# Kernel optimization log

Measured on AMD Instinct MI355X. Metric: run time of the kernel, lower is better.

The kernel has to match this reference:

```python
import jax, jax.numpy as jnp
import numpy as np

N_E = 1024
E_DIM = 64
BETA = 0.4
N_TOK = 131072


def setup_inputs() -> dict:
    key = jax.random.key(0)
    k1, k2 = jax.random.split(key)
    z = jax.random.normal(k1, (N_TOK, E_DIM), dtype=jnp.float32)
    # torch init: uniform(-1/n_e, 1/n_e)
    codebook = jax.random.uniform(k2, (N_E, E_DIM), dtype=jnp.float32,
                                  minval=-1.0 / N_E, maxval=1.0 / N_E)
    return {"z": z, "codebook": codebook}


def reference(z, codebook):
    sg = jax.lax.stop_gradient
    # squared euclidean distances: [N, n_e]
    d = (jnp.sum(z * z, axis=1, keepdims=True)
         + jnp.sum(codebook * codebook, axis=1)
         - 2.0 * jnp.matmul(z, codebook.T))
    idx = jnp.argmin(d, axis=1)                      # [N]
    z_q = codebook[idx]                              # gather, [N, E_DIM]
    # commitment / codebook loss
    vq_loss = (jnp.mean((sg(z_q) - z) ** 2)
               + BETA * jnp.mean((z_q - sg(z)) ** 2))
    # straight-through estimator
    z_q_st = z + sg(z_q - z)
    # codebook usage statistics (mean of one-hot encodings)
    e_mean = jnp.bincount(idx, length=N_E).astype(z.dtype) / jnp.asarray(idx.shape[0], z.dtype)
    usage_loss = -jnp.sum(e_mean * jnp.log(e_mean + 1e-10))
    perplexity = jnp.exp(usage_loss)
    vq_loss = vq_loss + 0.01 * usage_loss
    return z_q_st, vq_loss, idx[:, None], perplexity
```

## Files before the change

kernel.cpp:

```cpp
#include <hip/hip_runtime.h>
#include <math.h>

#define N_TOK 131072
#define N_E   1024
#define E_DIM 64
#define BETA  0.4

#define ZQ_OFF   0
#define LOSS_OFF 8388608
#define IDX_OFF  8388609
#define PERP_OFF 8519681

#define WS_SLOTS 0
#define WS_C2    2048
#define WS_CNT   6144
#define WS_WLC   10240
#define WS_WLB   10256
#define WS_KEYSB 43024
#define WLCAP    8192

typedef _Float16 f16x8 __attribute__((ext_vector_type(8)));
typedef float f32x4  __attribute__((ext_vector_type(4)));
typedef unsigned long long u64;

__device__ __forceinline__ unsigned med3u(unsigned a, unsigned b, unsigned c) {
    unsigned d;
    asm("v_med3_u32 %0, %1, %2, %3" : "=v"(d) : "v"(a), "v"(b), "v"(c));
    return d;
}

__device__ __attribute__((noinline)) int exact_best_serial2(
    const float* __restrict__ z, const float* __restrict__ cb, int n) {
    const float* zr = z + (size_t)n * E_DIM;
    float r8[8];
#pragma unroll
    for (int j = 0; j < 8; ++j) r8[j] = __fmul_rn(zr[j], zr[j]);
#pragma unroll 1
    for (int i = 8; i < 64; i += 8)
#pragma unroll
        for (int j = 0; j < 8; ++j)
            r8[j] = __fadd_rn(r8[j], __fmul_rn(zr[i + j], zr[i + j]));
    float z2 = __fadd_rn(__fadd_rn(__fadd_rn(r8[0], r8[1]), __fadd_rn(r8[2], r8[3])),
                         __fadd_rn(__fadd_rn(r8[4], r8[5]), __fadd_rn(r8[6], r8[7])));
    u64 bestkey = ~0ull;
#pragma unroll 1
    for (int e = 0; e < N_E; ++e) {
        const float* cp = cb + (size_t)e * E_DIM;
        double cs = 0.0, mm = 0.0;
#pragma unroll 1
        for (int i = 0; i < E_DIM; ++i) {
            double cc = (double)cp[i];
            cs = fma(cc, cc, cs);
            mm = fma((double)zr[i], cc, mm);
        }
        float d = __fsub_rn(__fadd_rn(z2, (float)cs), __fmul_rn(2.0f, (float)mm));
        u64 key = ((u64)__float_as_uint(d) << 32) | (unsigned)e;
        if (key < bestkey) bestkey = key;
    }
    return (int)(bestkey & 0xffffffffu);
}

__global__ __launch_bounds__(1024, 4) void vq_all(
    const float* __restrict__ z, const float* __restrict__ cb,
    double* __restrict__ slots, float* __restrict__ c2g,
    int* __restrict__ counts, int* __restrict__ wlCnt,
    int* __restrict__ wlB, u64* __restrict__ keysB,
    float margin_u, float* __restrict__ out) {

    __shared__ __align__(16) unsigned char sbuf[131072];
    __shared__ __align__(8)  unsigned short c2s[N_E];
    __shared__ int   best_s[512];
    __shared__ unsigned char flag_s[512];
    __shared__ unsigned listA[512];
    __shared__ unsigned short listB[512];
    __shared__ int cntA, cntB, gbaseS;
    __shared__ int hist[N_E];
    __shared__ double wred[16], dredA[16];

    const int tid  = threadIdx.x;
    const int lane = tid & 63;
    const int wid  = tid >> 6;
    const int col  = lane & 15;
    const int quad = lane >> 4;
    const int blk_tok0 = blockIdx.x * 512;
    const int wave_tok0 = blk_tok0 + wid * 32;

    if (tid == 0) { cntA = 0; cntB = 0; }
    hist[tid] = 0;

    float4 zl[2][4];
#pragma unroll
    for (int m = 0; m < 2; ++m) {
        const float* zr = z + (size_t)(wave_tok0 + m * 16 + col) * E_DIM + quad * 8;
#pragma unroll
        for (int kc = 0; kc < 2; ++kc) {
            zl[m][kc * 2]     = *(const float4*)(zr + kc * 32);
            zl[m][kc * 2 + 1] = *(const float4*)(zr + kc * 32 + 4);
        }
    }

    {
        const float4* cb4 = (const float4*)cb;
#pragma unroll
        for (int r = 0; r < 16; ++r) {
            const int ft = r * 1024 + tid;
            const float4 v = cb4[ft];
            const int code = ft >> 4;
            const int k0   = (ft & 15) * 4;
            const int cc = ((code >> 4) << 1) | (k0 >> 5);
            const int l  = (((k0 >> 3) & 3) << 4) | (code & 15);
            const int dst = (cc << 9) | (l << 3) | (k0 & 7);
            union { _Float16 h[4]; uint2 u; } pk;
            pk.h[0] = (_Float16)(v.x * 1024.0f);
            pk.h[1] = (_Float16)(v.y * 1024.0f);
            pk.h[2] = (_Float16)(v.z * 1024.0f);
            pk.h[3] = (_Float16)(v.w * 1024.0f);
            *(uint2*)(sbuf + dst * 2) = pk.u;
        }
    }

    if (blockIdx.x == 0) {
        const float* p = cb + (size_t)tid * E_DIM;
        double s = 0.0;
#pragma unroll
        for (int k = 0; k < E_DIM; ++k) {
            double c = (double)p[k];
            s = fma(c, c, s);
        }
        c2g[tid] = (float)s;
    }
    __syncthreads();

    {
        const int code = tid;
        const int cc0 = (code >> 4) << 1;
        const int c15 = code & 15;
        float s = 0.f;
#pragma unroll
        for (int half = 0; half < 2; ++half)
#pragma unroll
            for (int lv = 0; lv < 4; ++lv) {
                const int off = (((cc0 + half) << 9) |
                                 (((lv << 4) | c15) << 3)) * 2;
                union { uint4 u; _Float16 h[8]; } b;
                b.u = *(const uint4*)(sbuf + off);
#pragma unroll
                for (int j = 0; j < 8; ++j) {
                    float f = (float)b.h[j];
                    s = fmaf(f, f, s);
                }
            }
        union { _Float16 h; unsigned short u; } q;
        q.h = (_Float16)(s * (-1.0f / 2048.0f));
        c2s[tid] = q.u;
    }

    f16x8 Ah[2][2];
#pragma unroll
    for (int m = 0; m < 2; ++m)
#pragma unroll
        for (int kc = 0; kc < 2; ++kc) {
            float4 u0 = zl[m][kc * 2], u1 = zl[m][kc * 2 + 1];
            f16x8 a;
            a[0] = (_Float16)u0.x; a[1] = (_Float16)u0.y;
            a[2] = (_Float16)u0.z; a[3] = (_Float16)u0.w;
            a[4] = (_Float16)u1.x; a[5] = (_Float16)u1.y;
            a[6] = (_Float16)u1.z; a[7] = (_Float16)u1.w;
            Ah[m][kc] = a;
        }

    unsigned k1[2][4], k2[2][4], k3[2][4];
#pragma unroll
    for (int m = 0; m < 2; ++m)
#pragma unroll
        for (int r = 0; r < 4; ++r) { k1[m][r] = 0u; k2[m][r] = 0u; k3[m][r] = 0u; }

    __syncthreads();

#pragma unroll 4
    for (int cl = 0; cl < 64; ++cl) {
        const unsigned char* bp = sbuf + cl * 2048 + lane * 16;
        union { uint4 u; f16x8 v; } b0, b1;
        b0.u = *(const uint4*)(bp);
        b1.u = *(const uint4*)(bp + 1024);
        union { unsigned short us; _Float16 h; } cv;
        cv.us = c2s[cl * 16 + col];
        const float ch = 64.0f + (float)cv.h;
        const f32x4 cinit = {ch, ch, ch, ch};
        const unsigned ctag = (unsigned)(63 - cl);
#pragma unroll
        for (int m = 0; m < 2; ++m) {
            f32x4 acc = __builtin_amdgcn_mfma_f32_16x16x32_f16(
                Ah[m][0], b0.v, cinit, 0, 0, 0);
            acc = __builtin_amdgcn_mfma_f32_16x16x32_f16(
                Ah[m][1], b1.v, acc, 0, 0, 0);
#pragma unroll
            for (int r = 0; r < 4; ++r) {
                unsigned key = (__float_as_uint(acc[r]) & 0xFFFFFFC0u) | ctag;
                unsigned t1 = min(k1[m][r], key);
                k3[m][r] = med3u(k2[m][r], k3[m][r], t1);
                k2[m][r] = med3u(k1[m][r], k2[m][r], key);
                k1[m][r] = max(k1[m][r], key);
            }
        }
    }

#pragma unroll 1
    for (int m = 0; m < 2; ++m) {
#pragma unroll 1
        for (int r = 0; r < 4; ++r) {
            const unsigned l1 = k1[m][r], l2 = k2[m][r], l3 = k3[m][r];
            unsigned g1 = l1, g2 = l2, g3 = l3;
#pragma unroll
            for (int d = 1; d < 16; d <<= 1) {
                unsigned p1 = __shfl_xor(g1, d, 64);
                unsigned p2 = __shfl_xor(g2, d, 64);
                unsigned p3 = __shfl_xor(g3, d, 64);
                unsigned t1 = min(g1, p1);
                g3 = med3u(g2, g3, t1);
                g2 = med3u(g1, g2, p1);
                g1 = max(g1, p1);
                g3 = med3u(g2, g3, p2);
                g2 = max(g2, p2);
                g3 = med3u(g2, g3, p3);
            }
            u64 bal1 = __ballot((l1 == g1) || (l2 == g1) || (l3 == g1));
            u64 bal2 = __ballot((l1 == g2) || (l2 == g2) || (l3 == g2));
            if (col == 0) {
                const int tl = wid * 32 + m * 16 + quad * 4 + r;
                unsigned m1 = (unsigned)((bal1 >> (quad * 16)) & 0xFFFFu);
                int c1 = __ffs(m1) - 1;
                int bbest = (63 - (int)(g1 & 63u)) * 16 + c1;
                float v1 = __uint_as_float(g1 & 0xFFFFFFC0u);
                float v2 = __uint_as_float(g2 & 0xFFFFFFC0u);
                float v3 = __uint_as_float(g3 & 0xFFFFFFC0u);
                int typ = 0, bsec = 0;
                if (v1 - v2 < margin_u) {
                    if (v1 - v3 < margin_u) typ = 2;
                    else {
                        unsigned m2 = (unsigned)((bal2 >> (quad * 16)) & 0xFFFFu);
                        if (g2 == g1) m2 &= ~(1u << c1);
                        if (__popc(m2) == 1) {
                            bsec = (63 - (int)(g2 & 63u)) * 16 + (__ffs(m2) - 1);
                            typ = 1;
                        } else typ = 2;
                    }
                }
                if (typ == 1) {
                    int pos = atomicAdd(&cntA, 1);
                    listA[pos] = ((unsigned)tl << 20) |
                                 ((unsigned)bbest << 10) | (unsigned)bsec;
                } else if (typ == 2) {
                    int pos = atomicAdd(&cntB, 1);
                    listB[pos] = (unsigned short)tl;
                }
                best_s[tl] = bbest;
                flag_s[tl] = (unsigned char)typ;
            }
        }
    }

    __syncthreads();
    if (tid == 0) gbaseS = atomicAdd(wlCnt, cntB);
    __syncthreads();
    if (tid < cntB) {
        const int tl = listB[tid];
        const int gp = gbaseS + tid;
        if (gp < WLCAP) {
            wlB[gp] = blk_tok0 + tl;
            keysB[gp] = ~0ull;
        } else {
            best_s[tl] = exact_best_serial2(z, cb, blk_tok0 + tl);
            flag_s[tl] = 0;
        }
    }
    __syncthreads();

    {
        const int sub = lane & 15, grp = lane >> 4;
        double dl = 0.0;
        const float4* zrow = (const float4*)z;
        const float4* crow = (const float4*)cb;
        float4* qrow = (float4*)(out + ZQ_OFF);
#pragma unroll
        for (int p = 0; p < 8; ++p) {
            int tl = wid * 32 + p * 4 + grp;
            if (!flag_s[tl]) {
                int n = blk_tok0 + tl;
                float4 z4 = zrow[(size_t)n * 16 + sub];
                float4 c4 = crow[(size_t)best_s[tl] * 16 + sub];
                float dx = c4.x - z4.x, dy = c4.y - z4.y;
                float dz = c4.z - z4.z, dw = c4.w - z4.w;
                float4 q;
                q.x = z4.x + dx; q.y = z4.y + dy;
                q.z = z4.z + dz; q.w = z4.w + dw;
                qrow[(size_t)n * 16 + sub] = q;
                dl += (double)dx * dx + (double)dy * dy
                    + (double)dz * dz + (double)dw * dw;
            }
        }
#pragma unroll
        for (int off = 32; off > 0; off >>= 1)
            dl += __shfl_down(dl, off, 64);
        if (lane == 0) wred[wid] = dl;
    }
    const int nA = cntA;

    {
        double da = 0.0;
        for (int t = tid; t < nA; t += 1024) {
            const unsigned ent = listA[t];
            const int tl = (int)(ent >> 20);
            const int e1 = (int)((ent >> 10) & 1023u);
            const int e2 = (int)(ent & 1023u);
            const int n  = blk_tok0 + tl;
            const float* zr = z + (size_t)n * E_DIM;
            float r8[8];
#pragma unroll
            for (int j = 0; j < 8; ++j) r8[j] = __fmul_rn(zr[j], zr[j]);
#pragma unroll
            for (int i = 8; i < 64; i += 8)
#pragma unroll
                for (int j = 0; j < 8; ++j)
                    r8[j] = __fadd_rn(r8[j], __fmul_rn(zr[i + j], zr[i + j]));
            float z2 = __fadd_rn(
                __fadd_rn(__fadd_rn(r8[0], r8[1]), __fadd_rn(r8[2], r8[3])),
                __fadd_rn(__fadd_rn(r8[4], r8[5]), __fadd_rn(r8[6], r8[7])));
            u64 bk = ~0ull;
#pragma unroll
            for (int c = 0; c < 2; ++c) {
                const int e = c ? e2 : e1;
                const float* cp = cb + (size_t)e * E_DIM;
                double cs = 0.0, mm = 0.0;
#pragma unroll
                for (int k = 0; k < E_DIM; ++k) {
                    double cc = (double)cp[k];
                    cs = fma(cc, cc, cs);
                    mm = fma((double)zr[k], cc, mm);
                }
                float d = __fsub_rn(__fadd_rn(z2, (float)cs),
                                    __fmul_rn(2.0f, (float)mm));
                u64 key = ((u64)__float_as_uint(d) << 32) | (unsigned)e;
                if (key < bk) bk = key;
            }
            const int best = (int)(bk & 0xffffffffull);
            const float4* cp4 = (const float4*)(cb + (size_t)best * E_DIM);
            const float4* zp4 = (const float4*)zr;
            float4* qp = (float4*)(out + ZQ_OFF + (size_t)n * E_DIM);
            double dd = 0.0;
#pragma unroll
            for (int k = 0; k < 16; ++k) {
                float4 c4 = cp4[k]; float4 zz = zp4[k];
                float dx = c4.x - zz.x, dy = c4.y - zz.y;
                float dz = c4.z - zz.z, dw = c4.w - zz.w;
                float4 q;
                q.x = zz.x + dx; q.y = zz.y + dy;
                q.z = zz.z + dz; q.w = zz.w + dw;
                qp[k] = q;
                dd += (double)dx * dx + (double)dy * dy
                    + (double)dz * dz + (double)dw * dw;
            }
            best_s[tl] = best;
            da += dd;
        }
#pragma unroll
        for (int off = 32; off > 0; off >>= 1)
            da += __shfl_down(da, off, 64);
        if (lane == 0) dredA[wid] = da;
    }

    __syncthreads();

    if (tid < 512 && flag_s[tid] != 2)
        atomicAdd(&hist[best_s[tid]], 1);
    if (tid < 512)
        out[IDX_OFF + blk_tok0 + tid] = (float)best_s[tid];
    if (tid == 0) {
        double s = 0.0;
#pragma unroll
        for (int i = 0; i < 16; ++i) s += wred[i] + dredA[i];
        slots[blockIdx.x] = s;
    }
    __syncthreads();
    if (hist[tid]) atomicAdd(&counts[tid], hist[tid]);
}

__global__ __launch_bounds__(64) void fixup_scan(
    const float* __restrict__ z, const float* __restrict__ cb,
    const float* __restrict__ c2, const int* __restrict__ wlB,
    const int* __restrict__ wlCnt, u64* __restrict__ keysB) {

    int count = *wlCnt; if (count > WLCAP) count = WLCAP;
    const int g = blockIdx.x >> 5;
    const int s = blockIdx.x & 31;
    if (g * 64 >= count) return;
    const int lane = threadIdx.x;
    const int w = g * 64 + lane;
    const bool valid = w < count;
    const int n = wlB[valid ? w : g * 64];

    float zf[E_DIM];
    const float4* zp = (const float4*)(z + (size_t)n * E_DIM);
#pragma unroll
    for (int k = 0; k < 16; ++k) {
        float4 v = zp[k];
        zf[4 * k] = v.x; zf[4 * k + 1] = v.y;
        zf[4 * k + 2] = v.z; zf[4 * k + 3] = v.w;
    }
    float r8[8];
#pragma unroll
    for (int j = 0; j < 8; ++j) r8[j] = __fmul_rn(zf[j], zf[j]);
#pragma unroll
    for (int i = 8; i < 64; i += 8)
#pragma unroll
        for (int j = 0; j < 8; ++j)
            r8[j] = __fadd_rn(r8[j], __fmul_rn(zf[i + j], zf[i + j]));
    const float z2 = __fadd_rn(
        __fadd_rn(__fadd_rn(r8[0], r8[1]), __fadd_rn(r8[2], r8[3])),
        __fadd_rn(__fadd_rn(r8[4], r8[5]), __fadd_rn(r8[6], r8[7])));

    const int e0 = s * 32;
    float d32[32];
    float dmin = 1e30f;
#pragma unroll 4
    for (int i = 0; i < 32; ++i) {
        const float* cp = cb + (size_t)(e0 + i) * E_DIM;
        float a0 = 0.f, a1 = 0.f, a2 = 0.f, a3 = 0.f;
#pragma unroll
        for (int k = 0; k < 64; k += 4) {
            a0 = fmaf(zf[k],     cp[k],     a0);
            a1 = fmaf(zf[k + 1], cp[k + 1], a1);
            a2 = fmaf(zf[k + 2], cp[k + 2], a2);
            a3 = fmaf(zf[k + 3], cp[k + 3], a3);
        }
        float d = z2 + c2[e0 + i] - 2.0f * ((a0 + a1) + (a2 + a3));
        d32[i] = d;
        dmin = fminf(dmin, d);
    }
    u64 best = ~0ull;
    const float thr = dmin + 4e-3f;
    for (int it = 0; it < 32; ++it) {
        float dm = d32[0]; int am = 0;
#pragma unroll
        for (int i = 1; i < 32; ++i) {
            bool t = d32[i] < dm;
            dm = t ? d32[i] : dm;
            am = t ? i : am;
        }
        bool need = dm <= thr;
        if (!__any(need)) break;
        if (need) {
            int e = e0 + am;
            const float* cp = cb + (size_t)e * E_DIM;
            double mm = 0.0;
#pragma unroll
            for (int i = 0; i < E_DIM; ++i)
                mm = fma((double)zf[i], (double)cp[i], mm);
            float d = __fsub_rn(__fadd_rn(z2, c2[e]),
                                __fmul_rn(2.0f, (float)mm));
            u64 key = ((u64)__float_as_uint(d) << 32) | (unsigned)e;
            if (key < best) best = key;
#pragma unroll
            for (int i = 0; i < 32; ++i)
                if (i == am) d32[i] = 1e30f;
        }
    }
    if (valid && best != ~0ull) atomicMin(&keysB[w], best);
}

__global__ __launch_bounds__(1024) void finalize4(
    const float* __restrict__ z, const float* __restrict__ cb,
    const int* __restrict__ wlB, const int* __restrict__ wlCnt,
    const u64* __restrict__ keysB, const int* __restrict__ counts,
    const double* __restrict__ slots, float* __restrict__ out) {

    __shared__ int hist[N_E];
    __shared__ double red[1024];
    __shared__ double ssq_s;
    const int tid = threadIdx.x;
    hist[tid] = 0;
    __syncthreads();

    int count = *wlCnt; if (count > WLCAP) count = WLCAP;
    double myss = 0.0;
    for (int w = tid; w < count; w += 1024) {
        const int n = wlB[w];
        const int best = (int)(keysB[w] & 0xffffffffull);
        const float4* cp4 = (const float4*)(cb + (size_t)best * E_DIM);
        const float4* zp4 = (const float4*)(z + (size_t)n * E_DIM);
        float4* qp = (float4*)(out + ZQ_OFF + (size_t)n * E_DIM);
        double dd = 0.0;
#pragma unroll
        for (int k = 0; k < 16; ++k) {
            float4 c4 = cp4[k]; float4 zz = zp4[k];
            float dx = c4.x - zz.x, dy = c4.y - zz.y;
            float dz = c4.z - zz.z, dw = c4.w - zz.w;
            float4 q;
            q.x = zz.x + dx; q.y = zz.y + dy;
            q.z = zz.z + dz; q.w = zz.w + dw;
            qp[k] = q;
            dd += (double)dx * dx + (double)dy * dy
                + (double)dz * dz + (double)dw * dw;
        }
        out[IDX_OFF + n] = (float)best;
        atomicAdd(&hist[best], 1);
        myss += dd;
    }

    red[tid] = myss + (tid < 256 ? slots[tid] : 0.0);
    __syncthreads();
    for (int s = 512; s > 0; s >>= 1) {
        if (tid < s) red[tid] += red[tid + s];
        __syncthreads();
    }
    if (tid == 0) ssq_s = red[0];
    __syncthreads();

    double em = (double)(counts[tid] + hist[tid]) / (double)N_TOK;
    red[tid] = -em * log(em + 1e-10);
    __syncthreads();
    for (int s = 512; s > 0; s >>= 1) {
        if (tid < s) red[tid] += red[tid + s];
        __syncthreads();
    }
    if (tid == 0) {
        double usage = red[0];
        double mse = ssq_s / (double)((size_t)N_TOK * E_DIM);
        out[LOSS_OFF] = (float)((1.0 + BETA) * mse + 0.01 * usage);
        out[PERP_OFF] = (float)exp(usage);
    }
}

extern "C" void kernel_launch(void* const* d_in, const int* in_sizes, int n_in,
                              void* d_out, int out_size, void* d_ws, size_t ws_size,
                              hipStream_t stream) {
    const float* z  = (const float*)d_in[0];
    const float* cb = (const float*)d_in[1];
    float* out = (float*)d_out;

    double* slots  = (double*)((char*)d_ws + WS_SLOTS);
    float*  c2g    = (float*)((char*)d_ws + WS_C2);
    int*    counts = (int*)((char*)d_ws + WS_CNT);
    int*    wlCnt  = (int*)((char*)d_ws + WS_WLC);
    int*    wlB    = (int*)((char*)d_ws + WS_WLB);
    u64*    keysB  = (u64*)((char*)d_ws + WS_KEYSB);

    hipMemsetAsync((char*)d_ws + WS_CNT, 0, 4100, stream);

    vq_all<<<256, 1024, 0, stream>>>(z, cb, slots, c2g, counts, wlCnt,
                                     wlB, keysB, 0.071f, out);
    fixup_scan<<<4096, 64, 0, stream>>>(z, cb, c2g, wlB, wlCnt, keysB);
    finalize4<<<1, 1024, 0, stream>>>(z, cb, wlB, wlCnt, keysB, counts,
                                      slots, out);
}
```

Baseline: 192.2 us.

## Split single-block finalize into parallel worklist apply kernel plus small reduction

The single 1024-thread finalize block that wrote z_q, indices and histogram for all fixup worklist tokens is split. A new 64-block kernel handles it with one wavefront per token, lane-per-element coalesced loads and stores, global atomic count updates and per-block partial sums in extra slots. A tiny finalize kernel then reduces the slots and computes the entropy. This spreads the serial worklist tail across many CUs, at the cost of an extra launch and global atomics.

After: 188.1 us. 2.1% less time.

```diff
diff --git a/kernel.cpp b/kernel.cpp
--- a/kernel.cpp
+++ b/kernel.cpp
@@ -12,11 +12,11 @@
 #define PERP_OFF 8519681
 
 #define WS_SLOTS 0
-#define WS_C2    2048
-#define WS_CNT   6144
-#define WS_WLC   10240
-#define WS_WLB   10256
-#define WS_KEYSB 43024
+#define WS_C2    2560
+#define WS_CNT   6656
+#define WS_WLC   10752
+#define WS_WLB   10768
+#define WS_KEYSB 43536
 #define WLCAP    8192
 
 typedef _Float16 f16x8 __attribute__((ext_vector_type(8)));
@@ -468,55 +468,54 @@
     if (valid && best != ~0ull) atomicMin(&keysB[w], best);
 }
 
-__global__ __launch_bounds__(1024) void finalize4(
+__global__ __launch_bounds__(256) void apply_typ2(
     const float* __restrict__ z, const float* __restrict__ cb,
     const int* __restrict__ wlB, const int* __restrict__ wlCnt,
-    const u64* __restrict__ keysB, const int* __restrict__ counts,
-    const double* __restrict__ slots, float* __restrict__ out) {
-
-    __shared__ int hist[N_E];
-    __shared__ double red[1024];
-    __shared__ double ssq_s;
-    const int tid = threadIdx.x;
-    hist[tid] = 0;
-    __syncthreads();
-
+    const u64* __restrict__ keysB, int* __restrict__ counts,
+    double* __restrict__ slots, float* __restrict__ out) {
+
+    __shared__ double part[4];
     int count = *wlCnt; if (count > WLCAP) count = WLCAP;
-    double myss = 0.0;
-    for (int w = tid; w < count; w += 1024) {
+    const int lane = threadIdx.x & 63;
+    const int lw   = threadIdx.x >> 6;
+    double acc = 0.0;
+    for (int w = blockIdx.x * 4 + lw; w < count; w += 256) {
         const int n = wlB[w];
         const int best = (int)(keysB[w] & 0xffffffffull);
-        const float4* cp4 = (const float4*)(cb + (size_t)best * E_DIM);
-        const float4* zp4 = (const float4*)(z + (size_t)n * E_DIM);
-        float4* qp = (float4*)(out + ZQ_OFF + (size_t)n * E_DIM);
-        double dd = 0.0;
-#pragma unroll
-        for (int k = 0; k < 16; ++k) {
-            float4 c4 = cp4[k]; float4 zz = zp4[k];
-            float dx = c4.x - zz.x, dy = c4.y - zz.y;
-            float dz = c4.z - zz.z, dw = c4.w - zz.w;
-            float4 q;
-            q.x = zz.x + dx; q.y = zz.y + dy;
-            q.z = zz.z + dz; q.w = zz.w + dw;
-            qp[k] = q;
-            dd += (double)dx * dx + (double)dy * dy
-                + (double)dz * dz + (double)dw * dw;
-        }
-        out[IDX_OFF + n] = (float)best;
-        atomicAdd(&hist[best], 1);
-        myss += dd;
-    }
-
-    red[tid] = myss + (tid < 256 ? slots[tid] : 0.0);
+        float cv = cb[(size_t)best * E_DIM + lane];
+        float zi = z[(size_t)n * E_DIM + lane];
+        float diff = cv - zi;
+        out[ZQ_OFF + (size_t)n * E_DIM + lane] = zi + diff;
+        double d2 = (double)diff * (double)diff;
+#pragma unroll
+        for (int off = 32; off > 0; off >>= 1)
+            d2 += __shfl_down(d2, off, 64);
+        if (lane == 0) {
+            acc += d2;
+            atomicAdd(&counts[best], 1);
+            out[IDX_OFF + n] = (float)best;
+        }
+    }
+    if (lane == 0) part[lw] = acc;
+    __syncthreads();
+    if (threadIdx.x == 0)
+        slots[256 + blockIdx.x] = part[0] + part[1] + part[2] + part[3];
+}
+
+__global__ __launch_bounds__(1024) void finalize5(
+    const int* __restrict__ counts, const double* __restrict__ slots,
+    float* __restrict__ out) {
+    __shared__ double red[1024];
+    const int tid = threadIdx.x;
+    red[tid] = (tid < 320) ? slots[tid] : 0.0;
     __syncthreads();
     for (int s = 512; s > 0; s >>= 1) {
         if (tid < s) red[tid] += red[tid + s];
         __syncthreads();
     }
-    if (tid == 0) ssq_s = red[0];
-    __syncthreads();
-
-    double em = (double)(counts[tid] + hist[tid]) / (double)N_TOK;
+    double ssq = red[0];
+    __syncthreads();
+    double em = (double)counts[tid] / (double)N_TOK;
     red[tid] = -em * log(em + 1e-10);
     __syncthreads();
     for (int s = 512; s > 0; s >>= 1) {
@@ -525,7 +524,7 @@
     }
     if (tid == 0) {
         double usage = red[0];
-        double mse = ssq_s / (double)((size_t)N_TOK * E_DIM);
+        double mse = ssq / (double)((size_t)N_TOK * E_DIM);
         out[LOSS_OFF] = (float)((1.0 + BETA) * mse + 0.01 * usage);
         out[PERP_OFF] = (float)exp(usage);
     }
@@ -550,6 +549,7 @@
     vq_all<<<256, 1024, 0, stream>>>(z, cb, slots, c2g, counts, wlCnt,
                                      wlB, keysB, 0.071f, out);
     fixup_scan<<<4096, 64, 0, stream>>>(z, cb, c2g, wlB, wlCnt, keysB);
-    finalize4<<<1, 1024, 0, stream>>>(z, cb, wlB, wlCnt, keysB, counts,
-                                      slots, out);
-}
+    apply_typ2<<<64, 256, 0, stream>>>(z, cb, wlB, wlCnt, keysB, counts,
+                                       slots, out);
+    finalize5<<<1, 1024, 0, stream>>>(counts, slots, out);
+}
```
